# Optimization experiments

Measured on AMD Instinct MI355X. Metric: run time of the kernel, lower is better.

Reference implementation:

```python
import jax, jax.numpy as jnp
import numpy as np

B, L, D = 2, 2048, 2048
NH, NKV = 16, 8
HD = D // NH            # 128
GQ = NH // NKV          # queries per kv head
THETA = 10000.0
SCALE = HD ** -0.5


def rope_tables(seq_len, dim, theta):
    inv_freq = 1.0 / theta ** (jnp.arange(0, dim, 2, dtype=jnp.float32) / dim)
    t = jnp.arange(seq_len, dtype=jnp.float32)
    freqs = jnp.outer(t, inv_freq)              # [L, dim/2]
    emb = jnp.concatenate([freqs, freqs], -1)   # [L, dim]
    return jnp.cos(emb), jnp.sin(emb)


def rotate_half(x):
    x1, x2 = jnp.split(x, 2, axis=-1)
    return jnp.concatenate([-x2, x1], -1)


def setup_inputs() -> dict:
    key = jax.random.key(0)
    ks = jax.random.split(key, 5)
    s = 0.02
    return {
        "x": jax.random.normal(ks[0], (B, L, D), jnp.float32),
        "Wq": jax.random.normal(ks[1], (NH * HD, D), jnp.float32) * s,
        "Wk": jax.random.normal(ks[2], (NKV * HD, D), jnp.float32) * s,
        "Wv": jax.random.normal(ks[3], (NKV * HD, D), jnp.float32) * s,
        "Wo": jax.random.normal(ks[4], (D, D), jnp.float32) * s,
    }


def reference(x, Wq, Wk, Wv, Wo):
    b, l, d = x.shape
    q = (x @ Wq.T).reshape(b, l, NH, HD).transpose(0, 2, 1, 3)    # [B,NH,L,HD]
    k = (x @ Wk.T).reshape(b, l, NKV, HD).transpose(0, 2, 1, 3)   # [B,NKV,L,HD]
    v = (x @ Wv.T).reshape(b, l, NKV, HD).transpose(0, 2, 1, 3)

    cos, sin = rope_tables(l, HD, THETA)                           # [L,HD]
    q = q * cos + rotate_half(q) * sin
    k = k * cos + rotate_half(k) * sin

    # GQA without materializing expanded K/V: group queries per kv head
    qg = q.reshape(b, NKV, GQ, l, HD)
    scores = jnp.einsum('bgrld,bgmd->bgrlm', qg, k) * SCALE        # [B,NKV,GQ,L,L]
    causal = jnp.triu(jnp.ones((l, l), bool), k=1)
    scores = jnp.where(causal, -jnp.inf, scores)
    attn = jax.nn.softmax(scores.astype(jnp.float32), axis=-1).astype(q.dtype)
    out = jnp.einsum('bgrlm,bgmd->bgrld', attn, v)                 # [B,NKV,GQ,L,HD]
    out = out.reshape(b, NH, l, HD).transpose(0, 2, 1, 3).reshape(b, l, d)
    return out @ Wo.T
```

## Files before the change

### kernel.cpp

```cpp
#include <hip/hip_runtime.h>
#include <cmath>

using u16 = unsigned short;
typedef u16    u16x4  __attribute__((ext_vector_type(4)));
typedef u16    u16x8  __attribute__((ext_vector_type(8)));
typedef __bf16 bf16x8 __attribute__((ext_vector_type(8)));
typedef float  f32x4  __attribute__((ext_vector_type(4)));

constexpr int Bc  = 2;
constexpr int Lc  = 2048;
constexpr int Dc  = 2048;
constexpr int NHc = 16;
constexpr int NKVc= 8;
constexpr int HDc = 128;

__device__ __forceinline__ u16 f2b(float f) {
  union { float f; unsigned u; } v; v.f = f;
  unsigned r = v.u + 0x7FFFu + ((v.u >> 16) & 1u);
  return (u16)(r >> 16);
}
__device__ __forceinline__ u16 f2b_fast(float f) {
  union { float f; unsigned u; } v; v.f = f;
  return (u16)((v.u + 0x8000u) >> 16);
}
__device__ __forceinline__ float b2f(u16 s) {
  union { unsigned u; float f; } v; v.u = ((unsigned)s) << 16;
  return v.f;
}
__device__ __forceinline__ bf16x8 ld_frag(const u16* p) {
  u16x8 u = *(const u16x8*)p;
  return __builtin_bit_cast(bf16x8, u);
}
__device__ __forceinline__ void gld_lds16(u16* ldst, const u16* gsrc) {
  __builtin_amdgcn_global_load_lds(
      (const __attribute__((address_space(1))) void*)gsrc,
      (__attribute__((address_space(3))) void*)ldst, 16, 0, 0);
}

__global__ void cvt_f32_bf16(const float* __restrict__ src, u16* __restrict__ dst, int n) {
  int i = (blockIdx.x * blockDim.x + threadIdx.x) * 4;
  if (i >= n) return;
  float4 v = *(const float4*)&src[i];
  u16x4 o = { f2b(v.x), f2b(v.y), f2b(v.z), f2b(v.w) };
  *(u16x4*)&dst[i] = o;
}

__global__ void cvt_w3(const float* __restrict__ Wq, const float* __restrict__ Wk,
                       const float* __restrict__ Wv, u16* __restrict__ dst) {
  const int n1 = Dc * Dc;
  const int n2 = n1 + (NKVc*HDc) * Dc;
  const int n3 = n2 + (NKVc*HDc) * Dc;
  int i = (blockIdx.x * blockDim.x + threadIdx.x) * 4;
  if (i >= n3) return;
  const float* src; int off;
  if (i < n1)      { src = Wq; off = i; }
  else if (i < n2) { src = Wk; off = i - n1; }
  else             { src = Wv; off = i - n2; }
  float4 v = *(const float4*)&src[off];
  u16x4 o = { f2b(v.x), f2b(v.y), f2b(v.z), f2b(v.w) };
  *(u16x4*)&dst[i] = o;
}

template <int MODE>
__global__ __launch_bounds__(256) void gemm_lds(
    const u16* __restrict__ A, const u16* __restrict__ W,
    float* __restrict__ Cf, u16* __restrict__ Qp, u16* __restrict__ Kp, u16* __restrict__ Vtp,
    int M, int N, int K)
{
  __shared__ u16 lds[16384];
  u16* lA = lds;
  u16* lB = lds + 8192;
  const int tid  = threadIdx.x;
  const int wave = tid >> 6, lane = tid & 63;
  const int quad = lane >> 4, l16 = lane & 15;
  const int t7   = l16 & 7;
  const int m0 = blockIdx.y * 128, n0 = blockIdx.x * 128;
  const int mw = (wave >> 1) * 64, nw = (wave & 1) * 64;
  const int r8 = lane >> 3;
  const int cgl = (lane & 7) ^ r8;

  f32x4 acc[4][4];
#pragma unroll
  for (int i = 0; i < 4; ++i)
#pragma unroll
    for (int j = 0; j < 4; ++j) acc[i][j] = {0.f, 0.f, 0.f, 0.f};

  for (int kt = 0; kt < K; kt += 64) {
#pragma unroll
    for (int cc = 0; cc < 4; ++cc) {
      int c = wave + cc * 4;
      gld_lds16(&lA[c * 512], &A[(size_t)(m0 + 8 * c + r8) * K + kt + cgl * 8]);
      gld_lds16(&lB[c * 512], &W[(size_t)(n0 + 8 * c + r8) * K + kt + cgl * 8]);
    }
    __syncthreads();
#pragma unroll
    for (int s = 0; s < 2; ++s) {
      bf16x8 af[4], bf[4];
#pragma unroll
      for (int i = 0; i < 4; ++i)
        af[i] = ld_frag(&lA[(mw + i*16 + l16) * 64 + ((quad + 4*s) ^ t7) * 8]);
#pragma unroll
      for (int j = 0; j < 4; ++j)
        bf[j] = ld_frag(&lB[(nw + j*16 + l16) * 64 + ((quad + 4*s) ^ t7) * 8]);
#pragma unroll
      for (int i = 0; i < 4; ++i)
#pragma unroll
        for (int j = 0; j < 4; ++j)
          acc[i][j] = __builtin_amdgcn_mfma_f32_16x16x32_bf16(af[i], bf[j], acc[i][j], 0, 0, 0);
    }
    __syncthreads();
  }

  if constexpr (MODE == 1) {
#pragma unroll
    for (int i = 0; i < 4; ++i)
#pragma unroll
      for (int j = 0; j < 4; ++j)
#pragma unroll
        for (int r = 0; r < 4; ++r) {
          int m = m0 + mw + i*16 + quad*4 + r;
          int n = n0 + nw + j*16 + l16;
          Cf[(size_t)m * N + n] = acc[i][j][r];
        }
  } else {
    if (n0 < 3072) {
      u16* Cb; int ldc, nc0;
      if (n0 < 2048) { Cb = Qp; ldc = 2048; nc0 = n0; }
      else           { Cb = Kp; ldc = 1024; nc0 = n0 - 2048; }
#pragma unroll
      for (int i = 0; i < 4; ++i)
#pragma unroll
        for (int j = 0; j < 4; ++j)
#pragma unroll
          for (int r = 0; r < 4; ++r) {
            int m = m0 + mw + i*16 + quad*4 + r;
            int n = nc0 + nw + j*16 + l16;
            Cb[(size_t)m * ldc + n] = f2b(acc[i][j][r]);
          }
    } else {
#pragma unroll
      for (int i = 0; i < 4; ++i)
#pragma unroll
        for (int j = 0; j < 4; ++j)
#pragma unroll
          for (int r = 0; r < 4; ++r) {
            int l = mw + i*16 + quad*4 + r;
            int d = nw + j*16 + l16;
            int dp = d ^ (((l >> 3) & 15) << 3);
            lds[l * 128 + dp] = f2b(acc[i][j][r]);
          }
      __syncthreads();
      const int b   = m0 >> 11;
      const int hkv = (n0 - 3072) >> 7;
      const size_t vbase = (((size_t)b * NKVc + hkv) * HDc) * (size_t)Lc;
#pragma unroll
      for (int it = 0; it < 8; ++it) {
        int slot = tid + it * 256;
        int d  = slot & 127;
        int l8 = slot >> 7;
        u16x8 v;
#pragma unroll
        for (int e = 0; e < 8; ++e) {
          int l = l8 * 8 + e;
          v[e] = lds[l * 128 + (d ^ (((l >> 3) & 15) << 3))];
        }
        *(u16x8*)&Vtp[vbase + (size_t)d * Lc + (m0 & (Lc - 1)) + l8 * 8] = v;
      }
    }
  }
}

__global__ void rope2_kernel(u16* __restrict__ Qp, u16* __restrict__ Kp, float qs)
{
  const int nQ = Bc * Lc * NHc * 64;
  const int nT = nQ + Bc * Lc * NKVc * 64;
  int t = blockIdx.x * blockDim.x + threadIdx.x;
  if (t >= nT) return;
  u16* T; int nheads; float osc; int idx;
  if (t < nQ) { T = Qp; nheads = NHc;  osc = qs;  idx = t; }
  else        { T = Kp; nheads = NKVc; osc = 1.f; idx = t - nQ; }
  int d   = idx & 63;
  int h   = (idx >> 6) % nheads;
  int row = idx / (nheads * 64);
  int l   = row & (Lc - 1);
  float freq = exp2f((float)d * (-13.287712379549449f / 64.f));
  float ang  = (float)l * freq;
  float s, c;
  sincosf(ang, &s, &c);
  size_t base = (size_t)row * (nheads * 128) + h * 128;
  float x1 = b2f(T[base + d]);
  float x2 = b2f(T[base + d + 64]);
  T[base + d]      = f2b((x1 * c - x2 * s) * osc);
  T[base + d + 64] = f2b((x2 * c + x1 * s) * osc);
}

__global__ __launch_bounds__(512) void flash_kernel(
    const u16* __restrict__ Q, const u16* __restrict__ K, const u16* __restrict__ Vt,
    u16* __restrict__ O)
{
  __shared__ u16 smem[41984];
  const int tid  = threadIdx.x;
  const int wave = tid >> 6, lane = tid & 63;
  const int quad = lane >> 4, l16 = lane & 15;
  const int hw = wave >> 2, wr = wave & 3;
  const int bhkv = blockIdx.x;
  const int b = bhkv >> 3, hkv = bhkv & 7;
  const int h = hkv * 2 + hw;

  const size_t kbase = ((size_t)b * Lc) * (NKVc * HDc) + (size_t)hkv * HDc;
  const size_t vbase = (((size_t)b * NKVc + hkv) * HDc) * (size_t)Lc;

  const int kr8 = lane >> 4;
  const int kcl = lane & 15;
  const int vr16 = lane >> 3;
  const int vkl  = lane & 7;

  u16* sP_w = smem + 32768 + wave * 1152;

  for (int pass = 0; pass < 2; ++pass) {
    const int qt = (pass == 0) ? (31 - (int)blockIdx.y) : (int)blockIdx.y;
    const int q0 = qt * 64;

    __syncthreads();
#pragma unroll
    for (int i = 0; i < 4; ++i) {
      int g = tid + i * 512;
      int row = g >> 4, cg = g & 15;
      int qh = hkv * 2 + (row >> 6);
      int rr = row & 63;
      *(u16x8*)&smem[row * 128 + (cg ^ (row & 15)) * 8] =
          *(const u16x8*)&Q[((size_t)(b * Lc + q0 + rr)) * Dc + (size_t)qh * HDc + cg * 8];
    }
    __syncthreads();
    bf16x8 qf[4];
#pragma unroll
    for (int ks = 0; ks < 4; ++ks)
      qf[ks] = ld_frag(&smem[(hw*64 + wr*16 + l16) * 128 + ((ks*4 + quad) ^ l16) * 8]);
    __syncthreads();

#pragma unroll
    for (int i = 0; i < 2; ++i) {
      int c = wave + i * 8;
      int row = c * 4 + kr8;
      gld_lds16(smem + c * 512,
                &K[kbase + (size_t)row * (NKVc*HDc) + (size_t)(kcl ^ (row & 15)) * 8]);
    }
#pragma unroll
    for (int i = 0; i < 2; ++i) {
      int c = wave + i * 8;
      int d = c * 8 + vr16;
      gld_lds16(smem + 16384 + c * 512,
                &Vt[vbase + (size_t)d * Lc + (size_t)(vkl ^ (d & 7)) * 8]);
    }

    f32x4 acc_o[8];
#pragma unroll
    for (int i = 0; i < 8; ++i) acc_o[i] = {0.f, 0.f, 0.f, 0.f};
    float ps[4] = {0.f, 0.f, 0.f, 0.f};

    for (int kt = 0; kt <= qt; ++kt) {
      const int kOff  = (kt & 1) ? 8192 : 0;
      const int kOffN = (kt & 1) ? 0 : 8192;
      const int vOff  = (kt & 1) ? 24576 : 16384;
      const int vOffN = (kt & 1) ? 16384 : 24576;

      __asm__ volatile("s_waitcnt vmcnt(2)\n\ts_barrier" ::: "memory");

      if (kt < qt) {
#pragma unroll
        for (int i = 0; i < 2; ++i) {
          int c = wave + i * 8;
          int row = (kt + 1) * 64 + c * 4 + kr8;
          gld_lds16(smem + kOffN + c * 512,
                    &K[kbase + (size_t)row * (NKVc*HDc) + (size_t)(kcl ^ (row & 15)) * 8]);
        }
      }

      const u16* sKc = smem + kOff;
      f32x4 accs[4];
#pragma unroll
      for (int n = 0; n < 4; ++n) accs[n] = {0.f, 0.f, 0.f, 0.f};
#pragma unroll
      for (int ks = 0; ks < 4; ++ks)
#pragma unroll
        for (int n = 0; n < 4; ++n) {
          bf16x8 kf = ld_frag(&sKc[(n*16 + l16) * 128 + ((ks*4 + quad) ^ l16) * 8]);
          accs[n] = __builtin_amdgcn_mfma_f32_16x16x32_bf16(qf[ks], kf, accs[n], 0, 0, 0);
        }

      const int qrow = q0 + wr*16 + quad*4;
      if (kt == qt) {
#pragma unroll
        for (int n = 0; n < 4; ++n) {
          int kg = kt*64 + n*16 + l16;
#pragma unroll
          for (int r = 0; r < 4; ++r)
            if (kg > qrow + r) accs[n][r] = -INFINITY;
        }
      }
#pragma unroll
      for (int n = 0; n < 4; ++n)
#pragma unroll
        for (int r = 0; r < 4; ++r) {
          float p = exp2f(accs[n][r]);
          accs[n][r] = p;
          ps[r] += p;
        }

#pragma unroll
      for (int n = 0; n < 4; ++n)
#pragma unroll
        for (int r = 0; r < 4; ++r)
          sP_w[(quad*4 + r) * 72 + n*16 + l16] = f2b_fast(accs[n][r]);

      if (kt < qt)
        __asm__ volatile("s_waitcnt vmcnt(2) lgkmcnt(0)\n\ts_barrier" ::: "memory");
      else
        __asm__ volatile("s_waitcnt vmcnt(0) lgkmcnt(0)\n\ts_barrier" ::: "memory");

      if (kt < qt) {
#pragma unroll
        for (int i = 0; i < 2; ++i) {
          int c = wave + i * 8;
          int d = c * 8 + vr16;
          gld_lds16(smem + vOffN + c * 512,
                    &Vt[vbase + (size_t)d * Lc + (kt+1)*64 + (size_t)(vkl ^ (d & 7)) * 8]);
        }
      }

      const u16* sVc = smem + vOff;
#pragma unroll
      for (int s2 = 0; s2 < 2; ++s2) {
        bf16x8 pf = ld_frag(&sP_w[l16 * 72 + s2*32 + quad*8]);
#pragma unroll
        for (int di = 0; di < 8; ++di) {
          bf16x8 vf = ld_frag(&sVc[(di*16 + l16) * 64 + ((s2*4 + quad) ^ (l16 & 7)) * 8]);
          acc_o[di] = __builtin_amdgcn_mfma_f32_16x16x32_bf16(pf, vf, acc_o[di], 0, 0, 0);
        }
      }
    }

#pragma unroll
    for (int off = 1; off < 16; off <<= 1)
#pragma unroll
      for (int r = 0; r < 4; ++r) ps[r] += __shfl_xor(ps[r], off);
    float inv[4];
#pragma unroll
    for (int r = 0; r < 4; ++r) inv[r] = 1.0f / ps[r];

#pragma unroll
    for (int di = 0; di < 8; ++di)
#pragma unroll
      for (int r = 0; r < 4; ++r) {
        int qrow = q0 + wr*16 + quad*4 + r;
        int d = di*16 + l16;
        float v = acc_o[di][r] * inv[r];
        O[((size_t)(b * Lc + qrow)) * Dc + (size_t)h * HDc + d] = f2b(v);
      }
  }
}

extern "C" void kernel_launch(void* const* d_in, const int* in_sizes, int n_in,
                              void* d_out, int out_size, void* d_ws, size_t ws_size,
                              hipStream_t stream)
{
  const float* x  = (const float*)d_in[0];
  const float* Wq = (const float*)d_in[1];
  const float* Wk = (const float*)d_in[2];
  const float* Wv = (const float*)d_in[3];
  const float* Wo = (const float*)d_in[4];
  float* out = (float*)d_out;

  const int M = Bc * Lc;
  u16* ws = (u16*)d_ws;
  u16* xb   = ws;
  u16* Ow   = xb;
  u16* Wcat = ws + (size_t)8 * 1024 * 1024;
  u16* Wob  = Wcat;
  u16* Qw   = Wcat + (size_t)8 * 1024 * 1024;
  u16* Kw   = Qw   + (size_t)8 * 1024 * 1024;
  u16* Vt   = Kw   + (size_t)4 * 1024 * 1024;

  const int nx = M * Dc;
  const int nq = Dc * Dc;
  const int nw3 = nq + 2 * (NKVc*HDc) * Dc;
  cvt_f32_bf16<<<nx/1024, 256, 0, stream>>>(x, xb, nx);
  cvt_w3<<<nw3/1024, 256, 0, stream>>>(Wq, Wk, Wv, Wcat);

  gemm_lds<2><<<dim3(32, 32), 256, 0, stream>>>(xb, Wcat, nullptr, Qw, Kw, Vt, M, 4096, Dc);

  const float qs = 0.08838834764831845f * 1.4426950408889634f;
  const int nrope = M * (NHc + NKVc) * 64;
  rope2_kernel<<<(nrope + 255) / 256, 256, 0, stream>>>(Qw, Kw, qs);

  flash_kernel<<<dim3(Bc*NKVc, 16), 512, 0, stream>>>(Qw, Kw, Vt, Ow);

  cvt_f32_bf16<<<nq/1024, 256, 0, stream>>>(Wo, Wob, nq);
  gemm_lds<1><<<dim3(16, 32), 256, 0, stream>>>(Ow, Wob, out, nullptr, nullptr, nullptr, M, Dc, Dc);
}
```

Measured before the change: 331.6 us.

## Replace QKV GEMM with 256x256 tiled, 4-stage async-LDS pipelined kernel

Adds a dedicated QKV projection kernel that uses 256x256 output tiles across 8 waves. It stages K-slices of 32 through a 4-slot LDS ring with direct global-to-LDS loads and explicit vmcnt waits, and reorders block IDs so neighbouring blocks share data in L2. The aim is more data reuse per block and overlap of global loads with MFMA work, replacing the older 128x128 single-buffered GEMM. The cost is heavy register and LDS use (128KB LDS, 128 accumulator floats per lane), and the loop count is hardcoded to K=2048. The output-projection GEMM is split into its own unchanged kernel.

```diff
diff --git a/kernel.cpp b/kernel.cpp
--- a/kernel.cpp
+++ b/kernel.cpp
@@ -61,11 +61,132 @@
   *(u16x4*)&dst[i] = o;
 }
 
-template <int MODE>
-__global__ __launch_bounds__(256) void gemm_lds(
+__device__ __forceinline__ void stage_tile32(u16* lds, const u16* __restrict__ A,
+    const u16* __restrict__ W, int slot, int kt, int m0, int n0, int wave, int lane)
+{
+  const int srow = lane >> 2;
+  const int scg  = lane & 3;
+  const int skey = (lane >> 3) & 3;
+  const int sb   = slot * 16384;
+#pragma unroll
+  for (int i = 0; i < 2; ++i) {
+    int c = wave + i * 8;
+    int row = c * 16 + srow;
+    gld_lds16(&lds[sb + c * 512],
+              &A[(size_t)(m0 + row) * Dc + kt * 32 + (scg ^ skey) * 8]);
+    gld_lds16(&lds[sb + 8192 + c * 512],
+              &W[(size_t)(n0 + row) * Dc + kt * 32 + (scg ^ skey) * 8]);
+  }
+}
+
+__device__ __forceinline__ void compute_tile32(const u16* lds, int slot,
+    int wm, int wn, int quad, int l16, f32x4 acc[8][4])
+{
+  const u16* sA = lds + slot * 16384;
+  const u16* sB = sA + 8192;
+  const int pcg = (quad ^ ((l16 >> 1) & 3)) * 8;
+  bf16x8 af[8], bfr[4];
+#pragma unroll
+  for (int mi = 0; mi < 8; ++mi)
+    af[mi] = ld_frag(&sA[(wm * 128 + mi * 16 + l16) * 32 + pcg]);
+#pragma unroll
+  for (int ni = 0; ni < 4; ++ni)
+    bfr[ni] = ld_frag(&sB[(wn * 64 + ni * 16 + l16) * 32 + pcg]);
+  __builtin_amdgcn_s_setprio(1);
+#pragma unroll
+  for (int mi = 0; mi < 8; ++mi)
+#pragma unroll
+    for (int ni = 0; ni < 4; ++ni)
+      acc[mi][ni] = __builtin_amdgcn_mfma_f32_16x16x32_bf16(af[mi], bfr[ni], acc[mi][ni], 0, 0, 0);
+  __builtin_amdgcn_s_setprio(0);
+}
+
+__global__ __launch_bounds__(512, 2) void gemm256_qkv(
     const u16* __restrict__ A, const u16* __restrict__ W,
-    float* __restrict__ Cf, u16* __restrict__ Qp, u16* __restrict__ Kp, u16* __restrict__ Vtp,
-    int M, int N, int K)
+    u16* __restrict__ Qp, u16* __restrict__ Kp, u16* __restrict__ Vtp)
+{
+  __shared__ u16 lds[65536];
+  const int tid  = threadIdx.x;
+  const int wave = tid >> 6, lane = tid & 63;
+  const int quad = lane >> 4, l16 = lane & 15;
+  const int bid = blockIdx.x;
+  const int swz = (bid & 7) * 32 + (bid >> 3);
+  const int tx = swz & 15, ty = swz >> 4;
+  const int m0 = ty * 256, n0 = tx * 256;
+  const int wm = wave >> 2, wn = wave & 3;
+
+  f32x4 acc[8][4];
+#pragma unroll
+  for (int i = 0; i < 8; ++i)
+#pragma unroll
+    for (int j = 0; j < 4; ++j) acc[i][j] = {0.f, 0.f, 0.f, 0.f};
+
+  stage_tile32(lds, A, W, 0, 0, m0, n0, wave, lane);
+  stage_tile32(lds, A, W, 1, 1, m0, n0, wave, lane);
+  stage_tile32(lds, A, W, 2, 2, m0, n0, wave, lane);
+
+  for (int kt = 0; kt < 61; ++kt) {
+    __asm__ volatile("s_waitcnt vmcnt(8)\n\ts_barrier" ::: "memory");
+    stage_tile32(lds, A, W, (kt + 3) & 3, kt + 3, m0, n0, wave, lane);
+    compute_tile32(lds, kt & 3, wm, wn, quad, l16, acc);
+  }
+  __asm__ volatile("s_waitcnt vmcnt(8)\n\ts_barrier" ::: "memory");
+  compute_tile32(lds, 1, wm, wn, quad, l16, acc);
+  __asm__ volatile("s_waitcnt vmcnt(4)\n\ts_barrier" ::: "memory");
+  compute_tile32(lds, 2, wm, wn, quad, l16, acc);
+  __asm__ volatile("s_waitcnt vmcnt(0)\n\ts_barrier" ::: "memory");
+  compute_tile32(lds, 3, wm, wn, quad, l16, acc);
+
+  if (n0 < 3072) {
+    u16* Cb; int ldc, nc0;
+    if (n0 < 2048) { Cb = Qp; ldc = 2048; nc0 = n0; }
+    else           { Cb = Kp; ldc = 1024; nc0 = n0 - 2048; }
+#pragma unroll
+    for (int mi = 0; mi < 8; ++mi)
+#pragma unroll
+      for (int ni = 0; ni < 4; ++ni)
+#pragma unroll
+        for (int r = 0; r < 4; ++r) {
+          int m = m0 + wm * 128 + mi * 16 + quad * 4 + r;
+          int n = nc0 + wn * 64 + ni * 16 + l16;
+          Cb[(size_t)m * ldc + n] = f2b(acc[mi][ni][r]);
+        }
+  } else {
+    __syncthreads();
+#pragma unroll
+    for (int mi = 0; mi < 8; ++mi)
+#pragma unroll
+      for (int ni = 0; ni < 4; ++ni)
+#pragma unroll
+        for (int r = 0; r < 4; ++r) {
+          int l = wm * 128 + mi * 16 + quad * 4 + r;
+          int d = wn * 64 + ni * 16 + l16;
+          lds[l * 256 + (((d >> 3) ^ (l & 31)) << 3) + (d & 7)] = f2b(acc[mi][ni][r]);
+        }
+    __syncthreads();
+    const int b    = m0 >> 11;
+    const int hkv0 = (n0 - 3072) >> 7;
+#pragma unroll
+    for (int it = 0; it < 16; ++it) {
+      int sl = tid + it * 512;
+      int dl = sl >> 5;
+      int lc = (sl & 31) * 8;
+      u16x8 v;
+#pragma unroll
+      for (int e = 0; e < 8; ++e) {
+        int l = lc + e;
+        v[e] = lds[l * 256 + (((dl >> 3) ^ (l & 31)) << 3) + (dl & 7)];
+      }
+      const int hkv = hkv0 + (dl >> 7);
+      const int d   = dl & 127;
+      *(u16x8*)&Vtp[(((size_t)b * NKVc + hkv) * HDc + d) * (size_t)Lc + (m0 & (Lc - 1)) + lc] = v;
+    }
+  }
+}
+
+__global__ __launch_bounds__(256) void gemm_out(
+    const u16* __restrict__ A, const u16* __restrict__ W,
+    float* __restrict__ Cf, int M, int N, int K)
 {
   __shared__ u16 lds[16384];
   u16* lA = lds;
@@ -111,63 +232,16 @@
     __syncthreads();
   }
 
-  if constexpr (MODE == 1) {
-#pragma unroll
-    for (int i = 0; i < 4; ++i)
-#pragma unroll
-      for (int j = 0; j < 4; ++j)
-#pragma unroll
-        for (int r = 0; r < 4; ++r) {
-          int m = m0 + mw + i*16 + quad*4 + r;
-          int n = n0 + nw + j*16 + l16;
-          Cf[(size_t)m * N + n] = acc[i][j][r];
-        }
-  } else {
-    if (n0 < 3072) {
-      u16* Cb; int ldc, nc0;
-      if (n0 < 2048) { Cb = Qp; ldc = 2048; nc0 = n0; }
-      else           { Cb = Kp; ldc = 1024; nc0 = n0 - 2048; }
-#pragma unroll
-      for (int i = 0; i < 4; ++i)
-#pragma unroll
-        for (int j = 0; j < 4; ++j)
-#pragma unroll
-          for (int r = 0; r < 4; ++r) {
-            int m = m0 + mw + i*16 + quad*4 + r;
-            int n = nc0 + nw + j*16 + l16;
-            Cb[(size_t)m * ldc + n] = f2b(acc[i][j][r]);
-          }
-    } else {
-#pragma unroll
-      for (int i = 0; i < 4; ++i)
-#pragma unroll
-        for (int j = 0; j < 4; ++j)
-#pragma unroll
-          for (int r = 0; r < 4; ++r) {
-            int l = mw + i*16 + quad*4 + r;
-            int d = nw + j*16 + l16;
-            int dp = d ^ (((l >> 3) & 15) << 3);
-            lds[l * 128 + dp] = f2b(acc[i][j][r]);
-          }
-      __syncthreads();
-      const int b   = m0 >> 11;
-      const int hkv = (n0 - 3072) >> 7;
-      const size_t vbase = (((size_t)b * NKVc + hkv) * HDc) * (size_t)Lc;
-#pragma unroll
-      for (int it = 0; it < 8; ++it) {
-        int slot = tid + it * 256;
-        int d  = slot & 127;
-        int l8 = slot >> 7;
-        u16x8 v;
-#pragma unroll
-        for (int e = 0; e < 8; ++e) {
-          int l = l8 * 8 + e;
-          v[e] = lds[l * 128 + (d ^ (((l >> 3) & 15) << 3))];
-        }
-        *(u16x8*)&Vtp[vbase + (size_t)d * Lc + (m0 & (Lc - 1)) + l8 * 8] = v;
-      }
-    }
-  }
+#pragma unroll
+  for (int i = 0; i < 4; ++i)
+#pragma unroll
+    for (int j = 0; j < 4; ++j)
+#pragma unroll
+      for (int r = 0; r < 4; ++r) {
+        int m = m0 + mw + i*16 + quad*4 + r;
+        int n = n0 + nw + j*16 + l16;
+        Cf[(size_t)m * N + n] = acc[i][j][r];
+      }
 }
 
 __global__ void rope2_kernel(u16* __restrict__ Qp, u16* __restrict__ Kp, float qs)
@@ -387,7 +461,7 @@
   cvt_f32_bf16<<<nx/1024, 256, 0, stream>>>(x, xb, nx);
   cvt_w3<<<nw3/1024, 256, 0, stream>>>(Wq, Wk, Wv, Wcat);
 
-  gemm_lds<2><<<dim3(32, 32), 256, 0, stream>>>(xb, Wcat, nullptr, Qw, Kw, Vt, M, 4096, Dc);
+  gemm256_qkv<<<256, 512, 0, stream>>>(xb, Wcat, Qw, Kw, Vt);
 
   const float qs = 0.08838834764831845f * 1.4426950408889634f;
   const int nrope = M * (NHc + NKVc) * 64;
@@ -396,5 +470,5 @@
   flash_kernel<<<dim3(Bc*NKVc, 16), 512, 0, stream>>>(Qw, Kw, Vt, Ow);
 
   cvt_f32_bf16<<<nq/1024, 256, 0, stream>>>(Wo, Wob, nq);
-  gemm_lds<1><<<dim3(16, 32), 256, 0, stream>>>(Ow, Wob, out, nullptr, nullptr, nullptr, M, Dc, Dc);
-}
+  gemm_out<<<dim3(16, 32), 256, 0, stream>>>(Ow, Wob, out, M, Dc, Dc);
+}
```

Result: no change. 337.8 us (+1.8%).
